# Performance work log

Measured on AMD Instinct MI355X. Metric: run time of the kernel, lower is better.

Reference implementation:

```python
import jax, jax.numpy as jnp
import numpy as np
from jax import lax

WINDOW_SIZE = 11
SIGMA = 1.5
C1 = 0.01 ** 2
C2 = 0.03 ** 2


def _gaussian_window_2d(window_size, sigma):
    # matches torch.linspace(-ws//2+1, ws//2, ws) -> integers -5..5 for ws=11
    lo = -(window_size // 2) + 1 if window_size % 2 == 0 else -(window_size // 2)
    xs = np.linspace(-(window_size // 2) + 1 - (0 if window_size % 2 else 0), window_size // 2, window_size)
    # For ws=11: -(-11//2)+... torch computes linspace(-ws//2+1, ws//2, ws) with Python floor div:
    start = -(window_size // 2) if False else (-window_size) // 2 + 1
    xs = np.linspace(start, window_size // 2, window_size)
    g = np.exp(-(xs ** 2) / (2.0 * sigma ** 2))
    g = g / g.sum()
    w2d = np.outer(g, g).astype(np.float32)  # [ws, ws]
    return w2d


def _depthwise_conv(x, w2d, channel):
    # x: [B, C, H, W]; depthwise 'SAME' conv with shared gaussian kernel
    kernel = jnp.broadcast_to(jnp.asarray(w2d)[None, None], (channel, 1, w2d.shape[0], w2d.shape[1]))
    return lax.conv_general_dilated(
        x, kernel, window_strides=(1, 1), padding='SAME',
        feature_group_count=channel,
        dimension_numbers=('NCHW', 'OIHW', 'NCHW'))


def setup_inputs() -> dict:
    key = jax.random.key(0)
    k1, k2 = jax.random.split(key)
    img1 = jax.random.uniform(k1, (16, 3, 512, 512), dtype=jnp.float32)
    img2 = jax.random.uniform(k2, (16, 3, 512, 512), dtype=jnp.float32)
    return {"img1": img1, "img2": img2}


def reference(img1, img2):
    channel = img1.shape[1]
    w2d = _gaussian_window_2d(WINDOW_SIZE, SIGMA)

    mu1 = _depthwise_conv(img1, w2d, channel)
    mu2 = _depthwise_conv(img2, w2d, channel)
    sigma1_sq = _depthwise_conv(img1 * img1, w2d, channel) - mu1 * mu1
    sigma2_sq = _depthwise_conv(img2 * img2, w2d, channel) - mu2 * mu2
    sigma12 = _depthwise_conv(img1 * img2, w2d, channel) - mu1 * mu2

    ssim_map = ((2 * mu1 * mu2 + C1) * (2 * sigma12 + C2)) / (
        (mu1 * mu1 + mu2 * mu2 + C1) * (sigma1_sq + sigma2_sq + C2))
    return ssim_map.mean()
```

## Files before the change

kernel.cpp:

```cpp
#include <hip/hip_runtime.h>
#include <cstdint>

#define IMG_H 512
#define IMG_W 512
#define ROW_BYTES (IMG_W * 4)
#define NPLANES 48
#define PLANE_SZ (IMG_H * IMG_W)
#define N_ELEM (NPLANES * PLANE_SZ)

#define TILE_W 48
#define TILE_H 32
#define GX 11
#define GY 16
#define NBLOCKS (GX * GY * NPLANES)
#define NPART (NBLOCKS * 4)
#define VPITCH 59

#define SSIM_C1 1e-4f
#define SSIM_C2 9e-4f

typedef float v2f __attribute__((ext_vector_type(2)));

typedef int rsrc_t __attribute__((ext_vector_type(4)));
__device__ float
llvm_amdgcn_raw_buffer_load_fp32(rsrc_t srsrc, int voffset, int soffset,
                                 int glc_slc) __asm("llvm.amdgcn.raw.buffer.load.f32");

__device__ inline rsrc_t make_rsrc(const void* p, int bytes) {
    rsrc_t r;
    r.x = (int)(uint32_t)(uintptr_t)p;
    r.y = (int)((uintptr_t)p >> 32);
    r.z = bytes;
    r.w = 0x00020000;
    return r;
}

__global__ __launch_bounds__(256, 5) void ssim_tile_kernel(
    const float* __restrict__ img1, const float* __restrict__ img2,
    float* __restrict__ partials)
{
    __shared__ float4 vs[TILE_H][VPITCH];

    const float gw[11] = {0.00102838f, 0.00759876f, 0.03600077f, 0.10936069f,
                          0.21300553f, 0.26601172f, 0.21300553f, 0.10936069f,
                          0.03600077f, 0.00759876f, 0.00102838f};

    const int tid  = threadIdx.x;
    const int lane = tid & 63;
    const int wv   = tid >> 6;
    const int r0   = wv * 8;
    const int ox = blockIdx.x * TILE_W;
    const int oy = blockIdx.y * TILE_H;

    const float* p1 = img1 + (size_t)blockIdx.z * PLANE_SZ;
    const float* p2 = img2 + (size_t)blockIdx.z * PLANE_SZ;
    const rsrc_t rr1 = make_rsrc(p1, PLANE_SZ * 4);
    const rsrc_t rr2 = make_rsrc(p2, PLANE_SZ * 4);

    {
        const int srow0 = __builtin_amdgcn_readfirstlane(oy + r0 - 5);
        const int gcol = ox + lane - 5;
        const int coff = ((unsigned)gcol < (unsigned)IMG_W) ? (gcol * 4) : 0x48000000;

        float xs[18], ys[18];
        #pragma unroll
        for (int i = 0; i < 18; ++i) {
            const int soff = (srow0 + i) * ROW_BYTES;
            xs[i] = llvm_amdgcn_raw_buffer_load_fp32(rr1, coff, soff, 0);
            ys[i] = llvm_amdgcn_raw_buffer_load_fp32(rr2, coff, soff, 0);
        }

        v2f accP[8], accQ[8];
        #pragma unroll
        for (int o = 0; o < 8; ++o) { accP[o] = (v2f)(0.f); accQ[o] = (v2f)(0.f); }
        #pragma unroll
        for (int i = 0; i < 18; ++i) {
            v2f P; P.x = xs[i] + ys[i]; P.y = xs[i] - ys[i];
            const v2f Q = P * P;
            #pragma unroll
            for (int o = 0; o < 8; ++o) {
                const int k = i - o;
                if (k >= 0 && k <= 10) {
                    const v2f w2 = (v2f)(gw[k]);
                    accP[o] = __builtin_elementwise_fma(P, w2, accP[o]);
                    accQ[o] = __builtin_elementwise_fma(Q, w2, accQ[o]);
                }
            }
        }
        if (lane < 58) {
            #pragma unroll
            for (int o = 0; o < 8; ++o)
                vs[r0 + o][lane] = make_float4(accP[o].x, accP[o].y,
                                               accQ[o].x, accQ[o].y);
        }
    }

    float lsum = 0.f;
    {
        const int r  = r0 + (lane >> 3);
        const int c0 = (lane & 7) * 6;
        v2f mP[6], mQ[6];
        #pragma unroll
        for (int j = 0; j < 6; ++j) { mP[j] = (v2f)(0.f); mQ[j] = (v2f)(0.f); }
        #pragma unroll
        for (int t = 0; t < 16; ++t) {
            const float4 v = vs[r][c0 + t];
            v2f vP; vP.x = v.x; vP.y = v.y;
            v2f vQ; vQ.x = v.z; vQ.y = v.w;
            #pragma unroll
            for (int j = 0; j < 6; ++j) {
                const int k = t - j;
                if (k >= 0 && k <= 10) {
                    const v2f w2 = (v2f)(gw[k]);
                    mP[j] = __builtin_elementwise_fma(vP, w2, mP[j]);
                    mQ[j] = __builtin_elementwise_fma(vQ, w2, mQ[j]);
                }
            }
        }
        #pragma unroll
        for (int j = 0; j < 6; ++j) {
            if (ox + c0 + j < IMG_W) {
                const float mus = mP[j].x, mud = mP[j].y;
                const float es2 = mQ[j].x, ed2 = mQ[j].y;
                const float a = mus * mus, b = mud * mud;
                const float num1 = (a - b) * 0.5f + SSIM_C1;
                const float den1 = (a + b) * 0.5f + SSIM_C1;
                const float num2 = (es2 - ed2 - (a - b)) * 0.5f + SSIM_C2;
                const float den2 = (es2 + ed2 - (a + b)) * 0.5f + SSIM_C2;
                lsum += (num1 * num2) * __builtin_amdgcn_rcpf(den1 * den2);
            }
        }
    }

    #pragma unroll
    for (int off = 32; off > 0; off >>= 1)
        lsum += __shfl_down(lsum, off, 64);
    if (lane == 0) {
        const int bid = blockIdx.x + GX * (blockIdx.y + GY * blockIdx.z);
        partials[(bid << 2) | wv] = lsum;
    }
}

__global__ __launch_bounds__(1024) void ssim_finalize_kernel(
    const float* __restrict__ partials, float* __restrict__ out)
{
    __shared__ double wred[16];
    const int tid  = threadIdx.x;
    const int lane = tid & 63;
    const int wv   = tid >> 6;
    double s = 0.0;
    #pragma unroll
    for (int i = 0; i < 33; ++i)
        s += (double)partials[tid + i * 1024];
    #pragma unroll
    for (int off = 32; off > 0; off >>= 1)
        s += __shfl_down(s, off, 64);
    if (lane == 0) wred[wv] = s;
    __syncthreads();
    if (wv == 0) {
        double v = (lane < 16) ? wred[lane] : 0.0;
        v += __shfl_down(v, 8, 64);
        v += __shfl_down(v, 4, 64);
        v += __shfl_down(v, 2, 64);
        v += __shfl_down(v, 1, 64);
        if (lane == 0) out[0] = (float)(v / (double)N_ELEM);
    }
}

extern "C" void kernel_launch(void* const* d_in, const int* in_sizes, int n_in,
                              void* d_out, int out_size, void* d_ws, size_t ws_size,
                              hipStream_t stream)
{
    const float* img1 = (const float*)d_in[0];
    const float* img2 = (const float*)d_in[1];
    float* partials   = (float*)d_ws;
    float* out        = (float*)d_out;

    dim3 grid(GX, GY, NPLANES);
    ssim_tile_kernel<<<grid, dim3(256), 0, stream>>>(img1, img2, partials);
    ssim_finalize_kernel<<<1, dim3(1024), 0, stream>>>(partials, out);
}
```

Measured before the change: 136.5 us.

## Store vertical-pass intermediates as fp16 in LDS and raise occupancy

Vertical-pass results (sum, diff and their squares) are packed as two half2 values into a uint2 in shared memory instead of a float4, halving LDS footprint and traffic. Launch bounds raise the minimum blocks per SM from 5 to 8, and the packed v2f FMAs are replaced with scalar fmaf. Storing blurred sums and squared sums in half precision risks accuracy loss, especially in the variance terms computed by subtraction, and the scalar FMAs may lose the packed-math throughput.

```diff
diff --git a/kernel.cpp b/kernel.cpp
--- a/kernel.cpp
+++ b/kernel.cpp
@@ -1,4 +1,5 @@
 #include <hip/hip_runtime.h>
+#include <hip/hip_fp16.h>
 #include <cstdint>
 
 #define IMG_H 512
@@ -19,8 +20,6 @@
 #define SSIM_C1 1e-4f
 #define SSIM_C2 9e-4f
 
-typedef float v2f __attribute__((ext_vector_type(2)));
-
 typedef int rsrc_t __attribute__((ext_vector_type(4)));
 __device__ float
 llvm_amdgcn_raw_buffer_load_fp32(rsrc_t srsrc, int voffset, int soffset,
@@ -35,11 +34,11 @@
     return r;
 }
 
-__global__ __launch_bounds__(256, 5) void ssim_tile_kernel(
+__global__ __launch_bounds__(256, 8) void ssim_tile_kernel(
     const float* __restrict__ img1, const float* __restrict__ img2,
     float* __restrict__ partials)
 {
-    __shared__ float4 vs[TILE_H][VPITCH];
+    __shared__ uint2 vs[TILE_H][VPITCH];
 
     const float gw[11] = {0.00102838f, 0.00759876f, 0.03600077f, 0.10936069f,
                           0.21300553f, 0.26601172f, 0.21300553f, 0.10936069f,
@@ -70,28 +69,33 @@
             ys[i] = llvm_amdgcn_raw_buffer_load_fp32(rr2, coff, soff, 0);
         }
 
-        v2f accP[8], accQ[8];
+        float as[8], ad[8], as2[8], ad2[8];
         #pragma unroll
-        for (int o = 0; o < 8; ++o) { accP[o] = (v2f)(0.f); accQ[o] = (v2f)(0.f); }
+        for (int o = 0; o < 8; ++o) { as[o]=0.f; ad[o]=0.f; as2[o]=0.f; ad2[o]=0.f; }
         #pragma unroll
         for (int i = 0; i < 18; ++i) {
-            v2f P; P.x = xs[i] + ys[i]; P.y = xs[i] - ys[i];
-            const v2f Q = P * P;
+            const float s = xs[i] + ys[i], d = xs[i] - ys[i];
+            const float s2 = s * s, d2 = d * d;
             #pragma unroll
             for (int o = 0; o < 8; ++o) {
                 const int k = i - o;
                 if (k >= 0 && k <= 10) {
-                    const v2f w2 = (v2f)(gw[k]);
-                    accP[o] = __builtin_elementwise_fma(P, w2, accP[o]);
-                    accQ[o] = __builtin_elementwise_fma(Q, w2, accQ[o]);
+                    const float w = gw[k];
+                    as[o]  = fmaf(w, s,  as[o]);
+                    ad[o]  = fmaf(w, d,  ad[o]);
+                    as2[o] = fmaf(w, s2, as2[o]);
+                    ad2[o] = fmaf(w, d2, ad2[o]);
                 }
             }
         }
         if (lane < 58) {
             #pragma unroll
-            for (int o = 0; o < 8; ++o)
-                vs[r0 + o][lane] = make_float4(accP[o].x, accP[o].y,
-                                               accQ[o].x, accQ[o].y);
+            for (int o = 0; o < 8; ++o) {
+                const __half2 hP = __floats2half2_rn(as[o],  ad[o]);
+                const __half2 hQ = __floats2half2_rn(as2[o], ad2[o]);
+                vs[r0 + o][lane] = make_uint2(__builtin_bit_cast(unsigned, hP),
+                                              __builtin_bit_cast(unsigned, hQ));
+            }
         }
     }
 
@@ -99,29 +103,31 @@
     {
         const int r  = r0 + (lane >> 3);
         const int c0 = (lane & 7) * 6;
-        v2f mP[6], mQ[6];
+        float ms[6], md[6], ms2[6], md2[6];
         #pragma unroll
-        for (int j = 0; j < 6; ++j) { mP[j] = (v2f)(0.f); mQ[j] = (v2f)(0.f); }
+        for (int j = 0; j < 6; ++j) { ms[j]=0.f; md[j]=0.f; ms2[j]=0.f; md2[j]=0.f; }
         #pragma unroll
         for (int t = 0; t < 16; ++t) {
-            const float4 v = vs[r][c0 + t];
-            v2f vP; vP.x = v.x; vP.y = v.y;
-            v2f vQ; vQ.x = v.z; vQ.y = v.w;
+            const uint2 w2 = vs[r][c0 + t];
+            const float2 vP = __half22float2(__builtin_bit_cast(__half2, w2.x));
+            const float2 vQ = __half22float2(__builtin_bit_cast(__half2, w2.y));
             #pragma unroll
             for (int j = 0; j < 6; ++j) {
                 const int k = t - j;
                 if (k >= 0 && k <= 10) {
-                    const v2f w2 = (v2f)(gw[k]);
-                    mP[j] = __builtin_elementwise_fma(vP, w2, mP[j]);
-                    mQ[j] = __builtin_elementwise_fma(vQ, w2, mQ[j]);
+                    const float w = gw[k];
+                    ms[j]  = fmaf(w, vP.x, ms[j]);
+                    md[j]  = fmaf(w, vP.y, md[j]);
+                    ms2[j] = fmaf(w, vQ.x, ms2[j]);
+                    md2[j] = fmaf(w, vQ.y, md2[j]);
                 }
             }
         }
         #pragma unroll
         for (int j = 0; j < 6; ++j) {
             if (ox + c0 + j < IMG_W) {
-                const float mus = mP[j].x, mud = mP[j].y;
-                const float es2 = mQ[j].x, ed2 = mQ[j].y;
+                const float mus = ms[j], mud = md[j];
+                const float es2 = ms2[j], ed2 = md2[j];
                 const float a = mus * mus, b = mud * mud;
                 const float num1 = (a - b) * 0.5f + SSIM_C1;
                 const float den1 = (a + b) * 0.5f + SSIM_C1;
```

After: 137.7 us. No clear change (+0.9%).

## Compute separable Gaussian convolutions with fp16 MFMA banded-matrix products

Applied to the files above, without the earlier changes.

Replaces the scalar FMA vertical and horizontal passes with 16x16x32 fp16 MFMA instructions, multiplying by a banded Gaussian weight matrix built in shared memory. Each wave now handles a 16-row by 64-column strip, streamed in 16-column chunks with vertical and horizontal passes interleaved through a small fp16 shared buffer. The aim is to move the convolution arithmetic off the vector ALUs onto the matrix cores and to shrink the halo overhead by using 64x64 tiles. It trades fp32 accuracy for fp16 inputs and intermediates, with a rescale for the rounded weight sum, which risks precision error in the variance terms.

```diff
diff --git a/kernel.cpp b/kernel.cpp
--- a/kernel.cpp
+++ b/kernel.cpp
@@ -8,20 +8,22 @@
 #define PLANE_SZ (IMG_H * IMG_W)
 #define N_ELEM (NPLANES * PLANE_SZ)
 
-#define TILE_W 48
-#define TILE_H 32
-#define GX 11
-#define GY 16
-#define NBLOCKS (GX * GY * NPLANES)
+#define GXB 8
+#define GYB 8
+#define NBLOCKS (GXB * GYB * NPLANES)
 #define NPART (NBLOCKS * 4)
-#define VPITCH 59
 
 #define SSIM_C1 1e-4f
 #define SSIM_C2 9e-4f
 
-typedef float v2f __attribute__((ext_vector_type(2)));
+#define PITCH 40
+#define CH_STRIDE (16 * PITCH)
+#define WV_STRIDE (4 * CH_STRIDE)
 
+typedef _Float16 f16x8 __attribute__((ext_vector_type(8)));
+typedef float f32x4 __attribute__((ext_vector_type(4)));
 typedef int rsrc_t __attribute__((ext_vector_type(4)));
+
 __device__ float
 llvm_amdgcn_raw_buffer_load_fp32(rsrc_t srsrc, int voffset, int soffset,
                                  int glc_slc) __asm("llvm.amdgcn.raw.buffer.load.f32");
@@ -35,108 +37,117 @@
     return r;
 }
 
-__global__ __launch_bounds__(256, 5) void ssim_tile_kernel(
+__global__ __launch_bounds__(256, 4) void ssim_tile_kernel(
     const float* __restrict__ img1, const float* __restrict__ img2,
     float* __restrict__ partials)
 {
-    __shared__ float4 vs[TILE_H][VPITCH];
-
-    const float gw[11] = {0.00102838f, 0.00759876f, 0.03600077f, 0.10936069f,
-                          0.21300553f, 0.26601172f, 0.21300553f, 0.10936069f,
-                          0.03600077f, 0.00759876f, 0.00102838f};
+    __shared__ __align__(16) _Float16 wtab[512];
+    __shared__ __align__(16) _Float16 vsum[4 * WV_STRIDE];
 
     const int tid  = threadIdx.x;
     const int lane = tid & 63;
     const int wv   = tid >> 6;
-    const int r0   = wv * 8;
-    const int ox = blockIdx.x * TILE_W;
-    const int oy = blockIdx.y * TILE_H;
+    const int n    = lane & 15;
+    const int q    = lane >> 4;
 
+    const float gwc[11] = {0.00102838f, 0.00759876f, 0.03600077f, 0.10936069f,
+                           0.21300553f, 0.26601172f, 0.21300553f, 0.10936069f,
+                           0.03600077f, 0.00759876f, 0.00102838f};
+
+    for (int idx = tid; idx < 512; idx += 256) {
+        const int l = idx >> 3, j = idx & 7;
+        const int d = ((l >> 4) * 8 + j) - (l & 15);
+        wtab[idx] = (_Float16)((d >= 0 && d <= 10) ? gwc[d] : 0.0f);
+    }
+    __syncthreads();
+    const f16x8 wfrag = *(const f16x8*)(wtab + lane * 8);
+
+    float S = 0.f;
+    #pragma unroll
+    for (int k = 0; k < 11; ++k) S += (float)(_Float16)gwc[k];
+    const float rs = 1.0f / (S * S);
+
+    const int C0 = blockIdx.x * 64;
+    const int R0 = blockIdx.y * 64 + wv * 16;
     const float* p1 = img1 + (size_t)blockIdx.z * PLANE_SZ;
     const float* p2 = img2 + (size_t)blockIdx.z * PLANE_SZ;
     const rsrc_t rr1 = make_rsrc(p1, PLANE_SZ * 4);
     const rsrc_t rr2 = make_rsrc(p2, PLANE_SZ * 4);
 
-    {
-        const int srow0 = __builtin_amdgcn_readfirstlane(oy + r0 - 5);
-        const int gcol = ox + lane - 5;
-        const int coff = ((unsigned)gcol < (unsigned)IMG_W) ? (gcol * 4) : 0x48000000;
+    const int rowterm = (R0 - 5 + q * 8) * ROW_BYTES;
+    _Float16* vbase = vsum + wv * WV_STRIDE;
+    float lsum = 0.f;
 
-        float xs[18], ys[18];
+    auto do_V = [&](int t) {
+        const int col  = C0 - 5 + 16 * t + n;
+        const int coff = ((unsigned)col < (unsigned)IMG_W) ? (col * 4) : 0x48000000;
+        const int vb   = coff + rowterm;
+        float xs[8], ys[8];
         #pragma unroll
-        for (int i = 0; i < 18; ++i) {
-            const int soff = (srow0 + i) * ROW_BYTES;
-            xs[i] = llvm_amdgcn_raw_buffer_load_fp32(rr1, coff, soff, 0);
-            ys[i] = llvm_amdgcn_raw_buffer_load_fp32(rr2, coff, soff, 0);
+        for (int j = 0; j < 8; ++j) {
+            xs[j] = llvm_amdgcn_raw_buffer_load_fp32(rr1, vb + j * ROW_BYTES, 0, 0);
+            ys[j] = llvm_amdgcn_raw_buffer_load_fp32(rr2, vb + j * ROW_BYTES, 0, 0);
         }
+        f16x8 fS, fD, fS2, fD2;
+        #pragma unroll
+        for (int j = 0; j < 8; ++j) {
+            const float s = xs[j] + ys[j], d = xs[j] - ys[j];
+            fS[j]  = (_Float16)s;
+            fD[j]  = (_Float16)d;
+            fS2[j] = (_Float16)(s * s);
+            fD2[j] = (_Float16)(d * d);
+        }
+        const f32x4 z = {0.f, 0.f, 0.f, 0.f};
+        const f32x4 cS  = __builtin_amdgcn_mfma_f32_16x16x32_f16(wfrag, fS,  z, 0, 0, 0);
+        const f32x4 cD  = __builtin_amdgcn_mfma_f32_16x16x32_f16(wfrag, fD,  z, 0, 0, 0);
+        const f32x4 cS2 = __builtin_amdgcn_mfma_f32_16x16x32_f16(wfrag, fS2, z, 0, 0, 0);
+        const f32x4 cD2 = __builtin_amdgcn_mfma_f32_16x16x32_f16(wfrag, fD2, z, 0, 0, 0);
+        _Float16* wp = vbase + (q * 4) * PITCH + 16 * (t & 1) + n;
+        #pragma unroll
+        for (int r = 0; r < 4; ++r) {
+            wp[r * PITCH + 0 * CH_STRIDE] = (_Float16)cS[r];
+            wp[r * PITCH + 1 * CH_STRIDE] = (_Float16)cD[r];
+            wp[r * PITCH + 2 * CH_STRIDE] = (_Float16)cS2[r];
+            wp[r * PITCH + 3 * CH_STRIDE] = (_Float16)cD2[r];
+        }
+    };
 
-        v2f accP[8], accQ[8];
+    auto do_H = [&](int u) {
+        const int kbase = (16 * u + q * 8) & 31;
+        const _Float16* rp = vbase + n * PITCH + kbase;
+        const f16x8 aS  = *(const f16x8*)(rp + 0 * CH_STRIDE);
+        const f16x8 aD  = *(const f16x8*)(rp + 1 * CH_STRIDE);
+        const f16x8 aS2 = *(const f16x8*)(rp + 2 * CH_STRIDE);
+        const f16x8 aD2 = *(const f16x8*)(rp + 3 * CH_STRIDE);
+        const f32x4 z = {0.f, 0.f, 0.f, 0.f};
+        const f32x4 hS  = __builtin_amdgcn_mfma_f32_16x16x32_f16(aS,  wfrag, z, 0, 0, 0);
+        const f32x4 hD  = __builtin_amdgcn_mfma_f32_16x16x32_f16(aD,  wfrag, z, 0, 0, 0);
+        const f32x4 hS2 = __builtin_amdgcn_mfma_f32_16x16x32_f16(aS2, wfrag, z, 0, 0, 0);
+        const f32x4 hD2 = __builtin_amdgcn_mfma_f32_16x16x32_f16(aD2, wfrag, z, 0, 0, 0);
         #pragma unroll
-        for (int o = 0; o < 8; ++o) { accP[o] = (v2f)(0.f); accQ[o] = (v2f)(0.f); }
-        #pragma unroll
-        for (int i = 0; i < 18; ++i) {
-            v2f P; P.x = xs[i] + ys[i]; P.y = xs[i] - ys[i];
-            const v2f Q = P * P;
-            #pragma unroll
-            for (int o = 0; o < 8; ++o) {
-                const int k = i - o;
-                if (k >= 0 && k <= 10) {
-                    const v2f w2 = (v2f)(gw[k]);
-                    accP[o] = __builtin_elementwise_fma(P, w2, accP[o]);
-                    accQ[o] = __builtin_elementwise_fma(Q, w2, accQ[o]);
-                }
-            }
+        for (int r = 0; r < 4; ++r) {
+            const float mus = hS[r]  * rs, mud = hD[r]  * rs;
+            const float es2 = hS2[r] * rs, ed2 = hD2[r] * rs;
+            const float a = mus * mus, b = mud * mud;
+            const float num1 = (a - b) * 0.5f + SSIM_C1;
+            const float den1 = (a + b) * 0.5f + SSIM_C1;
+            const float num2 = (es2 - ed2 - (a - b)) * 0.5f + SSIM_C2;
+            const float den2 = (es2 + ed2 - (a + b)) * 0.5f + SSIM_C2;
+            lsum += (num1 * num2) * __builtin_amdgcn_rcpf(den1 * den2);
         }
-        if (lane < 58) {
-            #pragma unroll
-            for (int o = 0; o < 8; ++o)
-                vs[r0 + o][lane] = make_float4(accP[o].x, accP[o].y,
-                                               accQ[o].x, accQ[o].y);
-        }
-    }
+    };
 
-    float lsum = 0.f;
-    {
-        const int r  = r0 + (lane >> 3);
-        const int c0 = (lane & 7) * 6;
-        v2f mP[6], mQ[6];
-        #pragma unroll
-        for (int j = 0; j < 6; ++j) { mP[j] = (v2f)(0.f); mQ[j] = (v2f)(0.f); }
-        #pragma unroll
-        for (int t = 0; t < 16; ++t) {
-            const float4 v = vs[r][c0 + t];
-            v2f vP; vP.x = v.x; vP.y = v.y;
-            v2f vQ; vQ.x = v.z; vQ.y = v.w;
-            #pragma unroll
-            for (int j = 0; j < 6; ++j) {
-                const int k = t - j;
-                if (k >= 0 && k <= 10) {
-                    const v2f w2 = (v2f)(gw[k]);
-                    mP[j] = __builtin_elementwise_fma(vP, w2, mP[j]);
-                    mQ[j] = __builtin_elementwise_fma(vQ, w2, mQ[j]);
-                }
-            }
-        }
-        #pragma unroll
-        for (int j = 0; j < 6; ++j) {
-            if (ox + c0 + j < IMG_W) {
-                const float mus = mP[j].x, mud = mP[j].y;
-                const float es2 = mQ[j].x, ed2 = mQ[j].y;
-                const float a = mus * mus, b = mud * mud;
-                const float num1 = (a - b) * 0.5f + SSIM_C1;
-                const float den1 = (a + b) * 0.5f + SSIM_C1;
-                const float num2 = (es2 - ed2 - (a - b)) * 0.5f + SSIM_C2;
-                const float den2 = (es2 + ed2 - (a + b)) * 0.5f + SSIM_C2;
-                lsum += (num1 * num2) * __builtin_amdgcn_rcpf(den1 * den2);
-            }
-        }
-    }
+    do_V(0); do_V(1);
+    do_H(0); do_V(2);
+    do_H(1); do_V(3);
+    do_H(2); do_V(4);
+    do_H(3);
 
     #pragma unroll
     for (int off = 32; off > 0; off >>= 1)
         lsum += __shfl_down(lsum, off, 64);
     if (lane == 0) {
-        const int bid = blockIdx.x + GX * (blockIdx.y + GY * blockIdx.z);
+        const int bid = blockIdx.x + GXB * (blockIdx.y + GYB * blockIdx.z);
         partials[(bid << 2) | wv] = lsum;
     }
 }
@@ -150,7 +161,7 @@
     const int wv   = tid >> 6;
     double s = 0.0;
     #pragma unroll
-    for (int i = 0; i < 33; ++i)
+    for (int i = 0; i < 12; ++i)
         s += (double)partials[tid + i * 1024];
     #pragma unroll
     for (int off = 32; off > 0; off >>= 1)
@@ -176,7 +187,7 @@
     float* partials   = (float*)d_ws;
     float* out        = (float*)d_out;
 
-    dim3 grid(GX, GY, NPLANES);
+    dim3 grid(GXB, GYB, NPLANES);
     ssim_tile_kernel<<<grid, dim3(256), 0, stream>>>(img1, img2, partials);
     ssim_finalize_kernel<<<1, dim3(1024), 0, stream>>>(partials, out);
 }
```

New measurement: 137.4 us. No clear change (+0.7%).
